# Performance work log

Hardware: AMD Instinct MI355X
Metric: run time of the kernel (lower is better)

The kernel has to match this reference:

```python
import jax, jax.numpy as jnp
import numpy as np

B, DIM, H, W = 8, 48, 256, 256
LIF = 4
GROUPS = 24
EPS = 1e-5
SLOPE = 0.1   # LeakyReLU negative slope
GAMA = 1.0    # ZIF surrogate-gradient width


@jax.custom_vjp
def zif(x):
    # Heaviside spike with rectangular surrogate gradient (ZIF)
    return (x > 0).astype(x.dtype)

def _zif_fwd(x):
    return (x > 0).astype(x.dtype), x

def _zif_bwd(x, g):
    return (g * jnp.clip(GAMA - jnp.abs(x), 0.0, None) * (1.0 / (GAMA * GAMA)),)

zif.defvjp(_zif_fwd, _zif_bwd)


def group_norm(x, gamma, beta):
    b, c, h, w = x.shape
    xg = x.reshape(b, GROUPS, c // GROUPS, h, w)
    mu = xg.mean(axis=(2, 3, 4), keepdims=True)
    var = ((xg - mu) ** 2).mean(axis=(2, 3, 4), keepdims=True)
    xn = ((xg - mu) * jax.lax.rsqrt(var + EPS)).reshape(b, c, h, w)
    return xn * gamma[None, :, None, None] + beta[None, :, None, None]


def leaky(x):
    return jnp.where(x >= 0, x, SLOPE * x)


def conv1x1(x, w, b):
    # w: [out_c, in_c]
    return jnp.einsum('bchw,oc->bohw', x, w) + b[None, :, None, None]


def dwconv3x3(x, w, b):
    # w: [C, 1, 3, 3], depthwise
    y = jax.lax.conv_general_dilated(
        x, w, window_strides=(1, 1), padding='SAME',
        dimension_numbers=('NCHW', 'OIHW', 'NCHW'),
        feature_group_count=x.shape[1])
    return y + b[None, :, None, None]


def lif_spike(x, tau, vth, axis):
    # Chunk spatial axis into LIF time steps, run leaky integrate-and-fire,
    # concatenate spike trains back along the same axis.
    chunks = jnp.stack(jnp.split(x, LIF, axis=axis), axis=0)  # [T, B, C, h', w']

    def step(mem, xt):
        mem = mem * tau + xt
        s = zif(mem - vth)
        return mem * (1.0 - s), s

    _, spikes = jax.lax.scan(step, jnp.zeros_like(chunks[0]), chunks)
    return jnp.moveaxis(spikes, 0, axis).reshape(x.shape)


def setup_inputs() -> dict:
    key = jax.random.key(0)
    ks = jax.random.split(key, 8)

    def rn(k, shape, scale):
        return jax.random.normal(k, shape, dtype=jnp.float32) * scale

    ones_c = jnp.ones((DIM,), jnp.float32)
    zeros_c = jnp.zeros((DIM,), jnp.float32)
    inp = {
        'x': jax.random.normal(ks[0], (B, DIM, H, W), dtype=jnp.float32),
        'w1': rn(ks[1], (DIM, DIM), 0.1), 'b1': zeros_c,
        'wdw': rn(ks[2], (DIM, 1, 3, 3), 0.1), 'bdw': zeros_c,
        'w21': rn(ks[3], (DIM, DIM), 0.1), 'b21': zeros_c,
        'w22': rn(ks[4], (DIM, DIM), 0.1), 'b22': zeros_c,
        'w3': rn(ks[5], (DIM, DIM), 0.1), 'b3': zeros_c,
        'g1': ones_c, 'be1': zeros_c,
        'g2': ones_c, 'be2': zeros_c,
        'g3': ones_c, 'be3': zeros_c,
        'g4': ones_c, 'be4': zeros_c,
        'g5': ones_c, 'be5': zeros_c,
        'tau1': jnp.asarray(0.25, jnp.float32), 'vth1': jnp.asarray(0.25, jnp.float32),
        'tau2': jnp.asarray(0.25, jnp.float32), 'vth2': jnp.asarray(0.25, jnp.float32),
    }
    return inp


def reference(x, w1, b1, wdw, bdw, w21, b21, w22, b22, w3, b3,
              g1, be1, g2, be2, g3, be3, g4, be4, g5, be5,
              tau1, vth1, tau2, vth2):
    h = leaky(group_norm(conv1x1(x, w1, b1), g1, be1))
    h = leaky(group_norm(dwconv3x3(h, wdw, bdw), g2, be2))
    x_lr = lif_spike(h, tau1, vth1, axis=2)   # spikes over height chunks
    x_td = lif_spike(h, tau2, vth2, axis=3)   # spikes over width chunks
    x_lr = leaky(group_norm(conv1x1(x_lr, w21, b21), g4, be4))
    x_td = leaky(group_norm(conv1x1(x_td, w22, b22), g5, be5))
    s = group_norm(x_lr + x_td, g3, be3)
    return conv1x1(s, w3, b3)
```

## Files before the change

kernel.cpp:

```cpp
#include <hip/hip_runtime.h>

#define NB 8
#define NC 48
#define NHW 65536
#define NTOT (NB*NC*NHW)

typedef __attribute__((ext_vector_type(8))) short short8;
typedef __attribute__((ext_vector_type(4))) float f32x4;

__device__ __forceinline__ float lrelu(float v) { return v >= 0.0f ? v : 0.1f * v; }

__device__ __forceinline__ unsigned short f2bf(float f) {
    unsigned int u = __float_as_uint(f);
    return (unsigned short)((u + 0x7fffu + ((u >> 16) & 1u)) >> 16);
}
__device__ __forceinline__ float bf2f(unsigned short v) {
    return __uint_as_float((unsigned int)v << 16);
}

__global__ __launch_bounds__(256) void transpose_w1_kernel(
    const float* __restrict__ w1, float* __restrict__ wt)
{
    int i = blockIdx.x * 256 + threadIdx.x;
    if (i >= 2304) return;
    int o = i / 48, c = i % 48;
    wt[c * 48 + o] = w1[i];
}

__global__ __launch_bounds__(256) void pack_w2122_kernel(
    const float* __restrict__ w21, const float* __restrict__ w22,
    unsigned short* __restrict__ Wp)
{
    int i = blockIdx.x * 256 + threadIdx.x;
    if (i >= 6144) return;
    int m = i / 3072, e = i % 3072;
    int mt = e >> 10, r2 = e & 1023, ks = r2 >> 9, r3 = r2 & 511;
    int lane = r3 >> 3, j = r3 & 7;
    int o = mt * 16 + (lane & 15), c = ks * 32 + (lane >> 4) * 8 + j;
    const float* W = m ? w22 : w21;
    float v = (c < 48) ? W[o * 48 + c] : 0.f;
    Wp[i] = f2bf(v);
}

__global__ __launch_bounds__(256) void pack_w3_kernel(
    const float* __restrict__ w3, const float* __restrict__ sc3,
    const float* __restrict__ sh3, const float* __restrict__ b3,
    unsigned short* __restrict__ Wp3, float* __restrict__ b3f)
{
    int i = blockIdx.x * 256 + threadIdx.x;
    if (i < 24576) {
        int b = i / 3072, e = i % 3072;
        int mt = e >> 10, r2 = e & 1023, ks = r2 >> 9, r3 = r2 & 511;
        int lane = r3 >> 3, j = r3 & 7;
        int o = mt * 16 + (lane & 15), c = ks * 32 + (lane >> 4) * 8 + j;
        float v = (c < 48) ? w3[o * 48 + c] * sc3[b * 48 + c] : 0.f;
        Wp3[i] = f2bf(v);
    } else if (i < 24960) {
        int k = i - 24576;
        int b = k / 48, o = k % 48;
        float s = b3[o];
        for (int c = 0; c < 48; c++) s = fmaf(w3[o * 48 + c], sh3[b * 48 + c], s);
        b3f[k] = s;
    }
}

__global__ __launch_bounds__(256) void conv48f_kernel(
    const float* __restrict__ in, const float* __restrict__ Wt,
    const float* __restrict__ bias, float* __restrict__ out,
    float* __restrict__ partial)
{
    int tid  = threadIdx.x;
    int lane = tid & 63;
    int wid  = tid >> 6;
    int blk  = blockIdx.x;
    int b    = blk >> 8;
    int px0  = (blk & 255) * 256 + lane * 4;
    int ob   = __builtin_amdgcn_readfirstlane(wid * 12);

    size_t base = (size_t)b * NC * NHW + px0;

    float acc[12][4];
#pragma unroll
    for (int o = 0; o < 12; o++) {
        float bz = bias[ob + o];
#pragma unroll
        for (int j = 0; j < 4; j++) acc[o][j] = bz;
    }

#pragma unroll
    for (int c0 = 0; c0 < 48; c0 += 4) {
        float xv[4][4];
#pragma unroll
        for (int cc = 0; cc < 4; cc++) {
            float4 t = *(const float4*)(in + base + (size_t)(c0 + cc) * NHW);
            xv[cc][0] = t.x; xv[cc][1] = t.y; xv[cc][2] = t.z; xv[cc][3] = t.w;
        }
#pragma unroll
        for (int cc = 0; cc < 4; cc++) {
            const float* wrow = Wt + (c0 + cc) * 48 + ob;
#pragma unroll
            for (int o = 0; o < 12; o++) {
                float wv = wrow[o];
#pragma unroll
                for (int j = 0; j < 4; j++)
                    acc[o][j] = fmaf(xv[cc][j], wv, acc[o][j]);
            }
        }
    }

#pragma unroll
    for (int o = 0; o < 12; o++) {
        float4 t = {acc[o][0], acc[o][1], acc[o][2], acc[o][3]};
        *(float4*)(out + base + (size_t)(ob + o) * NHW) = t;
    }

#pragma unroll
    for (int i = 0; i < 6; i++) {
        float s = 0.f, q = 0.f;
#pragma unroll
        for (int k = 0; k < 2; k++)
#pragma unroll
            for (int j = 0; j < 4; j++) {
                float a = acc[2 * i + k][j];
                s += a;
                q = fmaf(a, a, q);
            }
#pragma unroll
        for (int off = 32; off; off >>= 1) {
            s += __shfl_down(s, off);
            q += __shfl_down(q, off);
        }
        if (lane == 0) {
            partial[(size_t)blk * 48 + ob + 2 * i]     = s;
            partial[(size_t)blk * 48 + ob + 2 * i + 1] = q;
        }
    }
}

__global__ __launch_bounds__(256) void dwconv_kernel(
    const float* __restrict__ in, const float* __restrict__ wdw,
    const float* __restrict__ bdw,
    const float* __restrict__ scale, const float* __restrict__ shift,
    float* __restrict__ out, float* __restrict__ partial)
{
    int tid = threadIdx.x;
    int blk = blockIdx.x;
    int bc  = blk >> 6;
    int rg  = blk & 63;
    int r   = tid >> 6;
    int w4  = tid & 63;
    int h   = rg * 4 + r;
    int c0  = w4 * 4;
    int c   = bc % 48;

    const float* plane = in + (size_t)bc * NHW;
    float sc = scale[bc], sh = shift[bc];

    float wk[9];
#pragma unroll
    for (int i = 0; i < 9; i++) wk[i] = wdw[c * 9 + i];
    float bv = bdw[c];

    float raw[3][6];
#pragma unroll
    for (int dy = 0; dy < 3; dy++) {
        int hh  = h + dy - 1;
        int hcl = min(max(hh, 0), 255);
        const float* row = plane + hcl * 256;
        float4 m  = *(const float4*)(row + c0);
        float lft = row[(w4 > 0) ? (c0 - 1) : 0];
        float rgt = row[(w4 < 63) ? (c0 + 4) : 255];
        raw[dy][0] = lft; raw[dy][1] = m.x; raw[dy][2] = m.y;
        raw[dy][3] = m.z; raw[dy][4] = m.w; raw[dy][5] = rgt;
    }

    float v[3][6];
#pragma unroll
    for (int dy = 0; dy < 3; dy++) {
        int hh = h + dy - 1;
        bool hv = (hh >= 0) && (hh < 256);
#pragma unroll
        for (int j = 0; j < 6; j++) {
            bool valid = hv && !(j == 0 && w4 == 0) && !(j == 5 && w4 == 63);
            float t = lrelu(fmaf(raw[dy][j], sc, sh));
            v[dy][j] = valid ? t : 0.f;
        }
    }

    float acc[4] = {bv, bv, bv, bv};
#pragma unroll
    for (int dy = 0; dy < 3; dy++)
#pragma unroll
        for (int dx = 0; dx < 3; dx++) {
            float wv = wk[dy * 3 + dx];
#pragma unroll
            for (int j = 0; j < 4; j++)
                acc[j] = fmaf(v[dy][j + dx], wv, acc[j]);
        }

    float4 o = {acc[0], acc[1], acc[2], acc[3]};
    *(float4*)(out + (size_t)bc * NHW + h * 256 + c0) = o;

    float s = (acc[0] + acc[1]) + (acc[2] + acc[3]);
    float q = fmaf(acc[0], acc[0], fmaf(acc[1], acc[1],
              fmaf(acc[2], acc[2], acc[3] * acc[3])));
#pragma unroll
    for (int off = 32; off; off >>= 1) {
        s += __shfl_down(s, off);
        q += __shfl_down(q, off);
    }
    __shared__ float red[8];
    int lane = tid & 63, wid = tid >> 6;
    if (lane == 0) { red[wid * 2] = s; red[wid * 2 + 1] = q; }
    __syncthreads();
    if (tid == 0) {
        partial[(size_t)blk * 2]     = red[0] + red[2] + red[4] + red[6];
        partial[(size_t)blk * 2 + 1] = red[1] + red[3] + red[5] + red[7];
    }
}

__global__ __launch_bounds__(256) void lif_fused_kernel(
    const float* __restrict__ in,
    const float* __restrict__ scale, const float* __restrict__ shift,
    const float* __restrict__ tau1p, const float* __restrict__ vth1p,
    const float* __restrict__ tau2p, const float* __restrict__ vth2p,
    unsigned char* __restrict__ spkH, unsigned char* __restrict__ spkW)
{
    int id  = blockIdx.x * 256 + threadIdx.x;
    int ww4 = id & 15;
    int hh  = (id >> 4) & 63;
    int bc  = id >> 10;

    float sc = scale[bc], sh = shift[bc];
    float tau1 = tau1p[0], vth1 = vth1p[0];
    float tau2 = tau2p[0], vth2 = vth2p[0];

    const float* plane = in + (size_t)bc * NHW;

    float v[4][4][4];
#pragma unroll
    for (int t = 0; t < 4; t++)
#pragma unroll
        for (int u = 0; u < 4; u++) {
            float4 x = *(const float4*)(plane + (hh + 64 * t) * 256 + 64 * u + ww4 * 4);
            v[t][u][0] = lrelu(fmaf(x.x, sc, sh));
            v[t][u][1] = lrelu(fmaf(x.y, sc, sh));
            v[t][u][2] = lrelu(fmaf(x.z, sc, sh));
            v[t][u][3] = lrelu(fmaf(x.w, sc, sh));
        }

    unsigned int oH[4][4], oW[4][4];
#pragma unroll
    for (int t = 0; t < 4; t++)
#pragma unroll
        for (int u = 0; u < 4; u++) { oH[t][u] = 0u; oW[t][u] = 0u; }

    {
        float mem[16];
#pragma unroll
        for (int k = 0; k < 16; k++) mem[k] = 0.f;
#pragma unroll
        for (int t = 0; t < 4; t++)
#pragma unroll
            for (int u = 0; u < 4; u++)
#pragma unroll
                for (int j = 0; j < 4; j++) {
                    float m = fmaf(mem[u * 4 + j], tau1, v[t][u][j]);
                    bool s = m > vth1;
                    oH[t][u] |= (s ? 1u : 0u) << (8 * j);
                    mem[u * 4 + j] = s ? 0.f : m;
                }
    }
    {
        float mem[16];
#pragma unroll
        for (int k = 0; k < 16; k++) mem[k] = 0.f;
#pragma unroll
        for (int u = 0; u < 4; u++)
#pragma unroll
            for (int t = 0; t < 4; t++)
#pragma unroll
                for (int j = 0; j < 4; j++) {
                    float m = fmaf(mem[t * 4 + j], tau2, v[t][u][j]);
                    bool s = m > vth2;
                    oW[t][u] |= (s ? 1u : 0u) << (8 * j);
                    mem[t * 4 + j] = s ? 0.f : m;
                }
    }

#pragma unroll
    for (int t = 0; t < 4; t++)
#pragma unroll
        for (int u = 0; u < 4; u++) {
            size_t off = (size_t)bc * NHW + (hh + 64 * t) * 256 + 64 * u + ww4 * 4;
            *(unsigned int*)(spkH + off) = oH[t][u];
            *(unsigned int*)(spkW + off) = oW[t][u];
        }
}

__global__ __launch_bounds__(256) void conv_mfma_u8_kernel(
    const unsigned char* __restrict__ in, const unsigned short* __restrict__ Wp,
    const float* __restrict__ bias, unsigned short* __restrict__ outp,
    float* __restrict__ P)
{
    __shared__ unsigned short Xs[64 * 260];
    __shared__ float red[4][96];

    int tid = threadIdx.x, lane = tid & 63, wid = tid >> 6;
    int l15 = lane & 15, g = lane >> 4;
    int blk = blockIdx.x, b = blk >> 8, pix0 = (blk & 255) * 256;

    {
        int px = (tid & 63) * 4;
        int cw = tid >> 6;
#pragma unroll
        for (int r = 0; r < 12; r++) {
            int c = r * 4 + cw;
            uchar4 v = *(const uchar4*)(in + ((size_t)(b * 48 + c) << 16) + pix0 + px);
            ushort4 u;
            u.x = v.x ? 0x3F80 : 0; u.y = v.y ? 0x3F80 : 0;
            u.z = v.z ? 0x3F80 : 0; u.w = v.w ? 0x3F80 : 0;
            *(ushort4*)&Xs[c * 260 + px] = u;
        }
        unsigned int* Xw = (unsigned int*)Xs;
        for (int i = tid; i < 2080; i += 256) Xw[6240 + i] = 0u;
    }
    __syncthreads();

    short8 af[3][2];
#pragma unroll
    for (int mt = 0; mt < 3; mt++)
#pragma unroll
        for (int ks = 0; ks < 2; ks++)
            af[mt][ks] = *(const short8*)(Wp + (mt * 2 + ks) * 512 + lane * 8);

    f32x4 acc[3][4];
#pragma unroll
    for (int mt = 0; mt < 3; mt++) {
        f32x4 bv = *(const f32x4*)(bias + mt * 16 + g * 4);
#pragma unroll
        for (int nt = 0; nt < 4; nt++) acc[mt][nt] = bv;
    }

#pragma unroll
    for (int nt = 0; nt < 4; nt++) {
        int pixl = wid * 64 + nt * 16 + l15;
#pragma unroll
        for (int ks = 0; ks < 2; ks++) {
            int rb = ks * 32 + g * 8;
            short8 bf;
#pragma unroll
            for (int j = 0; j < 8; j++) bf[j] = (short)Xs[(rb + j) * 260 + pixl];
#pragma unroll
            for (int mt = 0; mt < 3; mt++)
                acc[mt][nt] = __builtin_amdgcn_mfma_f32_16x16x32_bf16(
                    af[mt][ks], bf, acc[mt][nt], 0, 0, 0);
        }
    }

#pragma unroll
    for (int nt = 0; nt < 4; nt++) {
        int px = pix0 + wid * 64 + nt * 16 + l15;
        size_t obase = ((size_t)b * NHW + px) * 48;
#pragma unroll
        for (int mt = 0; mt < 3; mt++) {
            ushort4 o;
            o.x = f2bf(acc[mt][nt][0]); o.y = f2bf(acc[mt][nt][1]);
            o.z = f2bf(acc[mt][nt][2]); o.w = f2bf(acc[mt][nt][3]);
            *(ushort4*)(outp + obase + mt * 16 + g * 4) = o;
        }
    }

#pragma unroll
    for (int mt = 0; mt < 3; mt++) {
#pragma unroll
        for (int r = 0; r < 4; r++) {
            float sl = 0.f, sq = 0.f;
#pragma unroll
            for (int nt = 0; nt < 4; nt++) {
                float a = acc[mt][nt][r];
                sl += a;
                sq = fmaf(a, a, sq);
            }
#pragma unroll
            for (int off = 1; off < 16; off <<= 1) {
                sl += __shfl_xor(sl, off);
                sq += __shfl_xor(sq, off);
            }
            if (l15 == 0) {
                int ch = mt * 16 + g * 4 + r;
                red[wid][ch * 2]     = sl;
                red[wid][ch * 2 + 1] = sq;
            }
        }
    }
    __syncthreads();
    if (tid < 96)
        P[(size_t)blk * 96 + tid] = red[0][tid] + red[1][tid] + red[2][tid] + red[3][tid];
}

__global__ __launch_bounds__(256) void conv_mfma_f32out_kernel(
    const unsigned short* __restrict__ sp, const unsigned short* __restrict__ Wp3,
    const float* __restrict__ b3f, float* __restrict__ outp)
{
    int tid = threadIdx.x, lane = tid & 63, wid = tid >> 6;
    int l15 = lane & 15, g = lane >> 4;
    int blk = blockIdx.x, b = blk >> 8, pix0 = (blk & 255) * 256;

    const unsigned short* Wb = Wp3 + b * 3072;

    short8 af[3][2];
#pragma unroll
    for (int mt = 0; mt < 3; mt++)
#pragma unroll
        for (int ks = 0; ks < 2; ks++)
            af[mt][ks] = *(const short8*)(Wb + (mt * 2 + ks) * 512 + lane * 8);

    f32x4 acc[3][4];
#pragma unroll
    for (int mt = 0; mt < 3; mt++) {
        f32x4 bv = *(const f32x4*)(b3f + b * 48 + mt * 16 + g * 4);
#pragma unroll
        for (int nt = 0; nt < 4; nt++) acc[mt][nt] = bv;
    }

#pragma unroll
    for (int nt = 0; nt < 4; nt++) {
        int px = pix0 + wid * 64 + nt * 16 + l15;
        size_t pb = ((size_t)b * NHW + px) * 48;
#pragma unroll
        for (int ks = 0; ks < 2; ks++) {
            short8 bf = *(const short8*)(sp + pb + ks * 32 + g * 8);
#pragma unroll
            for (int mt = 0; mt < 3; mt++)
                acc[mt][nt] = __builtin_amdgcn_mfma_f32_16x16x32_bf16(
                    af[mt][ks], bf, acc[mt][nt], 0, 0, 0);
        }
    }

#pragma unroll
    for (int nt = 0; nt < 4; nt++) {
        int px = pix0 + wid * 64 + nt * 16 + l15;
#pragma unroll
        for (int mt = 0; mt < 3; mt++)
#pragma unroll
            for (int r = 0; r < 4; r++)
                outp[((size_t)(b * 48 + mt * 16 + g * 4 + r) << 16) + px] = acc[mt][nt][r];
    }
}

__global__ __launch_bounds__(256) void add_gn_nhwc_kernel(
    const unsigned short* __restrict__ a, const unsigned short* __restrict__ bb,
    const float* __restrict__ sc4, const float* __restrict__ sh4,
    const float* __restrict__ sc5, const float* __restrict__ sh5,
    unsigned short* __restrict__ o, float* __restrict__ P)
{
    __shared__ float red[4][96];
    int tid = threadIdx.x, lane = tid & 63, wid = tid >> 6;
    int g = lane >> 2, s = lane & 3, cs = s * 12;
    int blk = blockIdx.x;
    int pg = blk * 64 + wid * 16 + g;
    int b = pg >> 16;

    float sa[12], ha[12], sb[12], hb[12];
    {
        const f32x4* q;
        q = (const f32x4*)(sc4 + b * 48 + cs);
        f32x4 t0 = q[0], t1 = q[1], t2 = q[2];
#pragma unroll
        for (int i = 0; i < 4; i++) { sa[i] = t0[i]; sa[4 + i] = t1[i]; sa[8 + i] = t2[i]; }
        q = (const f32x4*)(sh4 + b * 48 + cs);
        t0 = q[0]; t1 = q[1]; t2 = q[2];
#pragma unroll
        for (int i = 0; i < 4; i++) { ha[i] = t0[i]; ha[4 + i] = t1[i]; ha[8 + i] = t2[i]; }
        q = (const f32x4*)(sc5 + b * 48 + cs);
        t0 = q[0]; t1 = q[1]; t2 = q[2];
#pragma unroll
        for (int i = 0; i < 4; i++) { sb[i] = t0[i]; sb[4 + i] = t1[i]; sb[8 + i] = t2[i]; }
        q = (const f32x4*)(sh5 + b * 48 + cs);
        t0 = q[0]; t1 = q[1]; t2 = q[2];
#pragma unroll
        for (int i = 0; i < 4; i++) { hb[i] = t0[i]; hb[4 + i] = t1[i]; hb[8 + i] = t2[i]; }
    }

    size_t base = (size_t)pg * 48 + cs;
    ushort4 A0 = *(const ushort4*)(a + base);
    ushort4 A1 = *(const ushort4*)(a + base + 4);
    ushort4 A2 = *(const ushort4*)(a + base + 8);
    ushort4 B0 = *(const ushort4*)(bb + base);
    ushort4 B1 = *(const ushort4*)(bb + base + 4);
    ushort4 B2 = *(const ushort4*)(bb + base + 8);

    unsigned short av[12] = {A0.x, A0.y, A0.z, A0.w, A1.x, A1.y, A1.z, A1.w,
                             A2.x, A2.y, A2.z, A2.w};
    unsigned short bv[12] = {B0.x, B0.y, B0.z, B0.w, B1.x, B1.y, B1.z, B1.w,
                             B2.x, B2.y, B2.z, B2.w};

    float tv[12];
    unsigned short ov[12];
#pragma unroll
    for (int i = 0; i < 12; i++) {
        float fa = bf2f(av[i]);
        float fb = bf2f(bv[i]);
        float t = lrelu(fmaf(fa, sa[i], ha[i])) + lrelu(fmaf(fb, sb[i], hb[i]));
        tv[i] = t;
        ov[i] = f2bf(t);
    }
    ushort4 O0 = {ov[0], ov[1], ov[2], ov[3]};
    ushort4 O1 = {ov[4], ov[5], ov[6], ov[7]};
    ushort4 O2 = {ov[8], ov[9], ov[10], ov[11]};
    *(ushort4*)(o + base)     = O0;
    *(ushort4*)(o + base + 4) = O1;
    *(ushort4*)(o + base + 8) = O2;

#pragma unroll
    for (int i = 0; i < 12; i++) {
        float ss = tv[i], qq = tv[i] * tv[i];
#pragma unroll
        for (int off = 32; off >= 4; off >>= 1) {
            ss += __shfl_down(ss, off);
            qq += __shfl_down(qq, off);
        }
        if (lane < 4) {
            red[wid][(cs + i) * 2]     = ss;
            red[wid][(cs + i) * 2 + 1] = qq;
        }
    }
    __syncthreads();
    if (tid < 96)
        P[(size_t)blk * 96 + tid] = red[0][tid] + red[1][tid] + red[2][tid] + red[3][tid];
}

__global__ __launch_bounds__(256) void reduce_chunked48_kernel(
    const float* __restrict__ P, const float* __restrict__ gamma,
    const float* __restrict__ beta,
    float* __restrict__ scale, float* __restrict__ shift)
{
    int b = blockIdx.x / 24, g = blockIdx.x % 24;
    int tid = threadIdx.x;
    double s = (double)P[(size_t)(b * 256 + tid) * 48 + 2 * g];
    double q = (double)P[(size_t)(b * 256 + tid) * 48 + 2 * g + 1];
    __shared__ double ls[256], lq[256];
    ls[tid] = s; lq[tid] = q;
    __syncthreads();
    for (int st = 128; st; st >>= 1) {
        if (tid < st) { ls[tid] += ls[tid + st]; lq[tid] += lq[tid + st]; }
        __syncthreads();
    }
    if (tid == 0) {
        double mu  = ls[0] / 131072.0;
        double var = lq[0] / 131072.0 - mu * mu;
        double rstd = 1.0 / sqrt(var + 1e-5);
#pragma unroll
        for (int j = 0; j < 2; j++) {
            int c = 2 * g + j;
            double scv = rstd * (double)gamma[c];
            scale[b * 48 + c] = (float)scv;
            shift[b * 48 + c] = (float)((double)beta[c] - mu * scv);
        }
    }
}

__global__ __launch_bounds__(256) void reduce_plane_kernel(
    const float* __restrict__ P, int chunks,
    const float* __restrict__ gamma, const float* __restrict__ beta,
    float* __restrict__ scale, float* __restrict__ shift)
{
    int b = blockIdx.x / 24, g = blockIdx.x % 24;
    int tid = threadIdx.x;
    double s = 0.0, q = 0.0;
    for (int i = tid; i < 2 * chunks; i += 256) {
        int j = (i >= chunks) ? 1 : 0;
        int k = i - j * chunks;
        const float* p = P + ((size_t)((b * 48 + 2 * g + j) * chunks + k)) * 2;
        s += (double)p[0];
        q += (double)p[1];
    }
    __shared__ double ls[256], lq[256];
    ls[tid] = s; lq[tid] = q;
    __syncthreads();
    for (int st = 128; st; st >>= 1) {
        if (tid < st) { ls[tid] += ls[tid + st]; lq[tid] += lq[tid + st]; }
        __syncthreads();
    }
    if (tid == 0) {
        double mu  = ls[0] / 131072.0;
        double var = lq[0] / 131072.0 - mu * mu;
        double rstd = 1.0 / sqrt(var + 1e-5);
#pragma unroll
        for (int j = 0; j < 2; j++) {
            int c = 2 * g + j;
            double scv = rstd * (double)gamma[c];
            scale[b * 48 + c] = (float)scv;
            shift[b * 48 + c] = (float)((double)beta[c] - mu * scv);
        }
    }
}

__global__ __launch_bounds__(256) void reduce_rows48_kernel(
    const float* __restrict__ P, int rows_per_b,
    const float* __restrict__ gamma, const float* __restrict__ beta,
    float* __restrict__ scale, float* __restrict__ shift)
{
    int b = blockIdx.x / 24, g = blockIdx.x % 24;
    int tid = threadIdx.x;
    double s = 0.0, q = 0.0;
    for (int r = tid; r < rows_per_b; r += 256) {
        const float* p = P + (size_t)(b * rows_per_b + r) * 96;
        s += (double)p[4 * g] + (double)p[4 * g + 2];
        q += (double)p[4 * g + 1] + (double)p[4 * g + 3];
    }
    __shared__ double ls[256], lq[256];
    ls[tid] = s; lq[tid] = q;
    __syncthreads();
    for (int st = 128; st; st >>= 1) {
        if (tid < st) { ls[tid] += ls[tid + st]; lq[tid] += lq[tid + st]; }
        __syncthreads();
    }
    if (tid == 0) {
        double mu  = ls[0] / 131072.0;
        double var = lq[0] / 131072.0 - mu * mu;
        double rstd = 1.0 / sqrt(var + 1e-5);
#pragma unroll
        for (int j = 0; j < 2; j++) {
            int c = 2 * g + j;
            double scv = rstd * (double)gamma[c];
            scale[b * 48 + c] = (float)scv;
            shift[b * 48 + c] = (float)((double)beta[c] - mu * scv);
        }
    }
}

extern "C" void kernel_launch(void* const* d_in, const int* in_sizes, int n_in,
                              void* d_out, int out_size, void* d_ws, size_t ws_size,
                              hipStream_t stream)
{
    const float* x    = (const float*)d_in[0];
    const float* w1   = (const float*)d_in[1];
    const float* b1   = (const float*)d_in[2];
    const float* wdw  = (const float*)d_in[3];
    const float* bdw  = (const float*)d_in[4];
    const float* w21  = (const float*)d_in[5];
    const float* b21  = (const float*)d_in[6];
    const float* w22  = (const float*)d_in[7];
    const float* b22  = (const float*)d_in[8];
    const float* w3   = (const float*)d_in[9];
    const float* b3   = (const float*)d_in[10];
    const float* g1   = (const float*)d_in[11];
    const float* be1  = (const float*)d_in[12];
    const float* g2   = (const float*)d_in[13];
    const float* be2  = (const float*)d_in[14];
    const float* g3   = (const float*)d_in[15];
    const float* be3  = (const float*)d_in[16];
    const float* g4   = (const float*)d_in[17];
    const float* be4  = (const float*)d_in[18];
    const float* g5   = (const float*)d_in[19];
    const float* be5  = (const float*)d_in[20];
    const float* tau1 = (const float*)d_in[21];
    const float* vth1 = (const float*)d_in[22];
    const float* tau2 = (const float*)d_in[23];
    const float* vth2 = (const float*)d_in[24];

    float* out = (float*)d_out;
    char*  ws  = (char*)d_ws;

    float*          A   = (float*)ws;
    unsigned short* Tb3 = (unsigned short*)ws;
    unsigned short* Tb4 = Tb3 + (size_t)NTOT;
    unsigned char*  D   = (unsigned char*)(ws + (size_t)NTOT * 4);
    unsigned char*  E   = D + NTOT;
    char* p = ws + (size_t)NTOT * 6;
    float* P1 = (float*)p;  p += (size_t)2048 * 48 * 4;
    float* P2 = (float*)p;  p += (size_t)24576 * 2 * 4;
    float* P4 = (float*)p;  p += (size_t)2048 * 96 * 4;
    float* P5 = (float*)p;  p += (size_t)2048 * 96 * 4;
    float* P6 = (float*)p;  p += (size_t)8192 * 96 * 4;
    float* sc1 = (float*)p; p += 384 * 4;  float* sh1 = (float*)p; p += 384 * 4;
    float* sc2 = (float*)p; p += 384 * 4;  float* sh2 = (float*)p; p += 384 * 4;
    float* sc3 = (float*)p; p += 384 * 4;  float* sh3 = (float*)p; p += 384 * 4;
    float* sc4 = (float*)p; p += 384 * 4;  float* sh4 = (float*)p; p += 384 * 4;
    float* sc5 = (float*)p; p += 384 * 4;  float* sh5 = (float*)p; p += 384 * 4;
    float*          Wt1  = (float*)p;          p += 2304 * 4;
    unsigned short* Wp2x = (unsigned short*)p; p += 6144 * 2;
    unsigned short* Wp3  = (unsigned short*)p; p += 24576 * 2;
    float*          b3f  = (float*)p;          p += 384 * 4;

    transpose_w1_kernel<<<9, 256, 0, stream>>>(w1, Wt1);
    pack_w2122_kernel<<<24, 256, 0, stream>>>(w21, w22, Wp2x);

    conv48f_kernel<<<2048, 256, 0, stream>>>(x, Wt1, b1, A, P1);
    reduce_chunked48_kernel<<<192, 256, 0, stream>>>(P1, g1, be1, sc1, sh1);

    dwconv_kernel<<<24576, 256, 0, stream>>>(A, wdw, bdw, sc1, sh1, out, P2);
    reduce_plane_kernel<<<192, 256, 0, stream>>>(P2, 64, g2, be2, sc2, sh2);

    lif_fused_kernel<<<1536, 256, 0, stream>>>(out, sc2, sh2, tau1, vth1, tau2, vth2, D, E);

    conv_mfma_u8_kernel<<<2048, 256, 0, stream>>>(D, Wp2x, b21, Tb3, P4);
    conv_mfma_u8_kernel<<<2048, 256, 0, stream>>>(E, Wp2x + 3072, b22, Tb4, P5);
    reduce_rows48_kernel<<<192, 256, 0, stream>>>(P4, 256, g4, be4, sc4, sh4);
    reduce_rows48_kernel<<<192, 256, 0, stream>>>(P5, 256, g5, be5, sc5, sh5);

    add_gn_nhwc_kernel<<<8192, 256, 0, stream>>>(Tb3, Tb4, sc4, sh4, sc5, sh5, Tb3, P6);
    reduce_rows48_kernel<<<192, 256, 0, stream>>>(P6, 1024, g3, be3, sc3, sh3);

    pack_w3_kernel<<<98, 256, 0, stream>>>(w3, sc3, sh3, b3, Wp3, b3f);
    conv_mfma_f32out_kernel<<<2048, 256, 0, stream>>>(Tb3, Wp3, b3f, out);
}
```

Before: 271.9 us.

## Merge small launches, double-buffer conv1 loads, hoist final conv B-fragment loads

```diff
diff --git a/kernel.cpp b/kernel.cpp
--- a/kernel.cpp
+++ b/kernel.cpp
@@ -18,28 +18,25 @@
     return __uint_as_float((unsigned int)v << 16);
 }
 
-__global__ __launch_bounds__(256) void transpose_w1_kernel(
-    const float* __restrict__ w1, float* __restrict__ wt)
+__global__ __launch_bounds__(256) void prep_kernel(
+    const float* __restrict__ w1, const float* __restrict__ w21,
+    const float* __restrict__ w22, float* __restrict__ Wt1,
+    unsigned short* __restrict__ Wp)
 {
     int i = blockIdx.x * 256 + threadIdx.x;
-    if (i >= 2304) return;
-    int o = i / 48, c = i % 48;
-    wt[c * 48 + o] = w1[i];
-}
-
-__global__ __launch_bounds__(256) void pack_w2122_kernel(
-    const float* __restrict__ w21, const float* __restrict__ w22,
-    unsigned short* __restrict__ Wp)
-{
-    int i = blockIdx.x * 256 + threadIdx.x;
-    if (i >= 6144) return;
-    int m = i / 3072, e = i % 3072;
-    int mt = e >> 10, r2 = e & 1023, ks = r2 >> 9, r3 = r2 & 511;
-    int lane = r3 >> 3, j = r3 & 7;
-    int o = mt * 16 + (lane & 15), c = ks * 32 + (lane >> 4) * 8 + j;
-    const float* W = m ? w22 : w21;
-    float v = (c < 48) ? W[o * 48 + c] : 0.f;
-    Wp[i] = f2bf(v);
+    if (i < 2304) {
+        int o = i / 48, c = i % 48;
+        Wt1[c * 48 + o] = w1[i];
+    } else if (i < 2304 + 6144) {
+        int e0 = i - 2304;
+        int m = e0 / 3072, e = e0 % 3072;
+        int mt = e >> 10, r2 = e & 1023, ks = r2 >> 9, r3 = r2 & 511;
+        int lane = r3 >> 3, j = r3 & 7;
+        int o = mt * 16 + (lane & 15), c = ks * 32 + (lane >> 4) * 8 + j;
+        const float* W = m ? w22 : w21;
+        float v = (c < 48) ? W[o * 48 + c] : 0.f;
+        Wp[e0] = f2bf(v);
+    }
 }
 
 __global__ __launch_bounds__(256) void pack_w3_kernel(
@@ -87,14 +84,27 @@
         for (int j = 0; j < 4; j++) acc[o][j] = bz;
     }
 
-#pragma unroll
-    for (int c0 = 0; c0 < 48; c0 += 4) {
-        float xv[4][4];
-#pragma unroll
-        for (int cc = 0; cc < 4; cc++) {
-            float4 t = *(const float4*)(in + base + (size_t)(c0 + cc) * NHW);
-            xv[cc][0] = t.x; xv[cc][1] = t.y; xv[cc][2] = t.z; xv[cc][3] = t.w;
-        }
+    float xv[2][4][4];
+#pragma unroll
+    for (int cc = 0; cc < 4; cc++) {
+        float4 t = *(const float4*)(in + base + (size_t)cc * NHW);
+        xv[0][cc][0] = t.x; xv[0][cc][1] = t.y;
+        xv[0][cc][2] = t.z; xv[0][cc][3] = t.w;
+    }
+
+#pragma unroll
+    for (int k = 0; k < 12; k++) {
+        const int cur = k & 1;
+        if (k < 11) {
+            int cn = (k + 1) * 4;
+#pragma unroll
+            for (int cc = 0; cc < 4; cc++) {
+                float4 t = *(const float4*)(in + base + (size_t)(cn + cc) * NHW);
+                xv[cur ^ 1][cc][0] = t.x; xv[cur ^ 1][cc][1] = t.y;
+                xv[cur ^ 1][cc][2] = t.z; xv[cur ^ 1][cc][3] = t.w;
+            }
+        }
+        int c0 = k * 4;
 #pragma unroll
         for (int cc = 0; cc < 4; cc++) {
             const float* wrow = Wt + (c0 + cc) * 48 + ob;
@@ -103,9 +113,10 @@
                 float wv = wrow[o];
 #pragma unroll
                 for (int j = 0; j < 4; j++)
-                    acc[o][j] = fmaf(xv[cc][j], wv, acc[o][j]);
+                    acc[o][j] = fmaf(xv[cur][cc][j], wv, acc[o][j]);
             }
         }
+        __builtin_amdgcn_sched_barrier(0);
     }
 
 #pragma unroll
@@ -299,16 +310,27 @@
 }
 
 __global__ __launch_bounds__(256) void conv_mfma_u8_kernel(
-    const unsigned char* __restrict__ in, const unsigned short* __restrict__ Wp,
-    const float* __restrict__ bias, unsigned short* __restrict__ outp,
-    float* __restrict__ P)
+    const unsigned char* __restrict__ in0, const unsigned char* __restrict__ in1,
+    const unsigned short* __restrict__ Wp,
+    const float* __restrict__ bias0, const float* __restrict__ bias1,
+    unsigned short* __restrict__ out0, unsigned short* __restrict__ out1,
+    float* __restrict__ P0, float* __restrict__ P1)
 {
     __shared__ unsigned short Xs[64 * 260];
     __shared__ float red[4][96];
 
     int tid = threadIdx.x, lane = tid & 63, wid = tid >> 6;
     int l15 = lane & 15, g = lane >> 4;
-    int blk = blockIdx.x, b = blk >> 8, pix0 = (blk & 255) * 256;
+    int blk2 = blockIdx.x;
+    int m    = blk2 >> 11;
+    int blk  = blk2 & 2047;
+    int b = blk >> 8, pix0 = (blk & 255) * 256;
+
+    const unsigned char*  in   = m ? in1 : in0;
+    const float*          bias = m ? bias1 : bias0;
+    unsigned short*       outp = m ? out1 : out0;
+    float*                P    = m ? P1 : P0;
+    const unsigned short* Wm   = Wp + m * 3072;
 
     {
         int px = (tid & 63) * 4;
@@ -332,7 +354,7 @@
     for (int mt = 0; mt < 3; mt++)
 #pragma unroll
         for (int ks = 0; ks < 2; ks++)
-            af[mt][ks] = *(const short8*)(Wp + (mt * 2 + ks) * 512 + lane * 8);
+            af[mt][ks] = *(const short8*)(Wm + (mt * 2 + ks) * 512 + lane * 8);
 
     f32x4 acc[3][4];
 #pragma unroll
@@ -409,6 +431,15 @@
 
     const unsigned short* Wb = Wp3 + b * 3072;
 
+    short8 bfr[4][2];
+#pragma unroll
+    for (int nt = 0; nt < 4; nt++) {
+        size_t pb = ((size_t)b * NHW + pix0 + wid * 64 + nt * 16 + l15) * 48;
+#pragma unroll
+        for (int ks = 0; ks < 2; ks++)
+            bfr[nt][ks] = *(const short8*)(sp + pb + ks * 32 + g * 8);
+    }
+
     short8 af[3][2];
 #pragma unroll
     for (int mt = 0; mt < 3; mt++)
@@ -425,18 +456,13 @@
     }
 
 #pragma unroll
-    for (int nt = 0; nt < 4; nt++) {
-        int px = pix0 + wid * 64 + nt * 16 + l15;
-        size_t pb = ((size_t)b * NHW + px) * 48;
-#pragma unroll
-        for (int ks = 0; ks < 2; ks++) {
-            short8 bf = *(const short8*)(sp + pb + ks * 32 + g * 8);
+    for (int nt = 0; nt < 4; nt++)
+#pragma unroll
+        for (int ks = 0; ks < 2; ks++)
 #pragma unroll
             for (int mt = 0; mt < 3; mt++)
                 acc[mt][nt] = __builtin_amdgcn_mfma_f32_16x16x32_bf16(
-                    af[mt][ks], bf, acc[mt][nt], 0, 0, 0);
-        }
-    }
+                    af[mt][ks], bfr[nt][ks], acc[mt][nt], 0, 0, 0);
 
 #pragma unroll
     for (int nt = 0; nt < 4; nt++) {
@@ -597,12 +623,22 @@
     }
 }
 
-__global__ __launch_bounds__(256) void reduce_rows48_kernel(
-    const float* __restrict__ P, int rows_per_b,
-    const float* __restrict__ gamma, const float* __restrict__ beta,
-    float* __restrict__ scale, float* __restrict__ shift)
-{
-    int b = blockIdx.x / 24, g = blockIdx.x % 24;
+__global__ __launch_bounds__(256) void reduce_rows48_dual_kernel(
+    const float* __restrict__ PA, const float* __restrict__ PB, int rows_per_b,
+    const float* __restrict__ gA, const float* __restrict__ beA,
+    const float* __restrict__ gB, const float* __restrict__ beB,
+    float* __restrict__ scA, float* __restrict__ shA,
+    float* __restrict__ scB, float* __restrict__ shB)
+{
+    int sel = blockIdx.x / 192;
+    int idx = blockIdx.x % 192;
+    const float* P     = sel ? PB : PA;
+    const float* gamma = sel ? gB : gA;
+    const float* beta  = sel ? beB : beA;
+    float* scale = sel ? scB : scA;
+    float* shift = sel ? shB : shA;
+
+    int b = idx / 24, g = idx % 24;
     int tid = threadIdx.x;
     double s = 0.0, q = 0.0;
     for (int r = tid; r < rows_per_b; r += 256) {
@@ -685,8 +721,7 @@
     unsigned short* Wp3  = (unsigned short*)p; p += 24576 * 2;
     float*          b3f  = (float*)p;          p += 384 * 4;
 
-    transpose_w1_kernel<<<9, 256, 0, stream>>>(w1, Wt1);
-    pack_w2122_kernel<<<24, 256, 0, stream>>>(w21, w22, Wp2x);
+    prep_kernel<<<33, 256, 0, stream>>>(w1, w21, w22, Wt1, Wp2x);
 
     conv48f_kernel<<<2048, 256, 0, stream>>>(x, Wt1, b1, A, P1);
     reduce_chunked48_kernel<<<192, 256, 0, stream>>>(P1, g1, be1, sc1, sh1);
@@ -696,13 +731,14 @@
 
     lif_fused_kernel<<<1536, 256, 0, stream>>>(out, sc2, sh2, tau1, vth1, tau2, vth2, D, E);
 
-    conv_mfma_u8_kernel<<<2048, 256, 0, stream>>>(D, Wp2x, b21, Tb3, P4);
-    conv_mfma_u8_kernel<<<2048, 256, 0, stream>>>(E, Wp2x + 3072, b22, Tb4, P5);
-    reduce_rows48_kernel<<<192, 256, 0, stream>>>(P4, 256, g4, be4, sc4, sh4);
-    reduce_rows48_kernel<<<192, 256, 0, stream>>>(P5, 256, g5, be5, sc5, sh5);
+    conv_mfma_u8_kernel<<<4096, 256, 0, stream>>>(
+        D, E, Wp2x, b21, b22, Tb3, Tb4, P4, P5);
+    reduce_rows48_dual_kernel<<<384, 256, 0, stream>>>(
+        P4, P5, 256, g4, be4, g5, be5, sc4, sh4, sc5, sh5);
 
     add_gn_nhwc_kernel<<<8192, 256, 0, stream>>>(Tb3, Tb4, sc4, sh4, sc5, sh5, Tb3, P6);
-    reduce_rows48_kernel<<<192, 256, 0, stream>>>(P6, 1024, g3, be3, sc3, sh3);
+    reduce_rows48_dual_kernel<<<192, 256, 0, stream>>>(
+        P6, P6, 1024, g3, be3, g3, be3, sc3, sh3, sc3, sh3);
 
     pack_w3_kernel<<<98, 256, 0, stream>>>(w3, sc3, sh3, b3, Wp3, b3f);
     conv_mfma_f32out_kernel<<<2048, 256, 0, stream>>>(Tb3, Wp3, b3f, out);
```

New measurement: 261.2 us. 1.04x faster.
